# Performance work log

Measured on AMD Instinct MI355X. Metric: run time of the kernel, lower is better.

Reference implementation:

```python
import jax, jax.numpy as jnp
import numpy as np
import math

EMBED = 1024
HEADS = 16
HEAD_DIM = EMBED // HEADS
B, Hh, Ww = 256, 10, 10
MAX_POS = 100


def setup_inputs() -> dict:
    key = jax.random.key(0)
    ks = jax.random.split(key, 10)
    s = 1.0 / math.sqrt(EMBED)
    return {
        "x": jax.random.normal(ks[0], (B, EMBED, Hh, Ww), dtype=jnp.float32),
        "Wq": jax.random.uniform(ks[1], (EMBED, EMBED), jnp.float32, -s, s),
        "bq": jax.random.uniform(ks[2], (EMBED,), jnp.float32, -s, s),
        "Wk": jax.random.uniform(ks[3], (EMBED, EMBED), jnp.float32, -s, s),
        "bk": jax.random.uniform(ks[4], (EMBED,), jnp.float32, -s, s),
        "Wv": jax.random.uniform(ks[5], (EMBED, EMBED), jnp.float32, -s, s),
        "bv": jax.random.uniform(ks[6], (EMBED,), jnp.float32, -s, s),
        "Wo": jax.random.uniform(ks[7], (EMBED, EMBED), jnp.float32, -s, s),
        "bo": jax.random.uniform(ks[8], (EMBED,), jnp.float32, -s, s),
        "pos_encoding": jax.random.normal(ks[9], (MAX_POS, EMBED), dtype=jnp.float32),
    }


def reference(x, Wq, bq, Wk, bk, Wv, bv, Wo, bo, pos_encoding):
    # x: [B, E, H, W]
    b, e, h, w = x.shape
    s = h * w  # seq_len
    scale = math.sqrt(HEAD_DIM)
    x_flat = x.reshape(b, e, s).transpose(0, 2, 1)  # [B, S, E]
    x_flat = x_flat + pos_encoding[:s][None]  # broadcast over batch
    q = x_flat @ Wq + bq
    k = x_flat @ Wk + bk
    v = x_flat @ Wv + bv
    # [B, H, S, D]
    q = q.reshape(b, s, HEADS, HEAD_DIM).transpose(0, 2, 1, 3)
    k = k.reshape(b, s, HEADS, HEAD_DIM).transpose(0, 2, 1, 3)
    v = v.reshape(b, s, HEADS, HEAD_DIM).transpose(0, 2, 1, 3)
    scores = jnp.einsum('bhqd,bhkd->bhqk', q, k) / scale
    attn = jax.nn.softmax(scores, axis=-1)  # dropout = identity (eval)
    attended = jnp.einsum('bhqk,bhkd->bhqd', attn, v)
    attended = attended.transpose(0, 2, 1, 3).reshape(b, s, e)
    out = attended @ Wo + bo
    out = out.transpose(0, 2, 1).reshape(b, e, h, w)
    return out, attn
```

## Files before the change

### kernel.cpp

```cpp
#include <hip/hip_runtime.h>

typedef unsigned short u16;
typedef __attribute__((ext_vector_type(8))) short short8;
typedef __attribute__((ext_vector_type(4))) float f32x4;

#define BATCH 256
#define S_LEN 100
#define EMB   1024
#define NHEAD 16
#define HDIM  64

__device__ __forceinline__ float b2f(u16 h) {
  union { unsigned u; float f; } v; v.u = ((unsigned)h) << 16; return v.f;
}
__device__ __forceinline__ u16 f2bf(float f) {
  union { float f; unsigned u; } v; v.f = f;
  unsigned r = v.u + 0x7fffu + ((v.u >> 16) & 1u);
  return (u16)(r >> 16);
}

__device__ __forceinline__ void gld_lds16(const u16* g, u16* l) {
  __builtin_amdgcn_global_load_lds((const __attribute__((address_space(1))) void*)g,
                                   (__attribute__((address_space(3))) void*)l,
                                   16, 0, 0);
}

__global__ __launch_bounds__(256) void w_xpose(
    const float* __restrict__ Wq, const float* __restrict__ Wk,
    const float* __restrict__ Wv, const float* __restrict__ Wo,
    u16* __restrict__ WtQ, u16* __restrict__ WtK,
    u16* __restrict__ WtV, u16* __restrict__ WtO)
{
  __shared__ u16 tile[64 * 73];
  int z = blockIdx.z;
  const float* W = (z == 0) ? Wq : (z == 1) ? Wk : (z == 2) ? Wv : Wo;
  u16* Wt        = (z == 0) ? WtQ : (z == 1) ? WtK : (z == 2) ? WtV : WtO;
  int k0 = blockIdx.x * 64, n0 = blockIdx.y * 64;
  for (int idx = threadIdx.x; idx < 4096; idx += 256) {
    int r = idx >> 6, c = idx & 63;
    tile[r * 73 + c] = f2bf(W[(size_t)(k0 + r) * EMB + n0 + c]);
  }
  __syncthreads();
  for (int idx = threadIdx.x; idx < 4096; idx += 256) {
    int c = idx >> 6, r = idx & 63;
    Wt[(size_t)(n0 + c) * EMB + k0 + r] = tile[r * 73 + c];
  }
}

__global__ __launch_bounds__(256) void xpose_pos(
    const float* __restrict__ x, const float* __restrict__ pos, u16* __restrict__ xT)
{
  __shared__ float tile[64 * 105];
  int e0 = blockIdx.x * 64;
  int b  = blockIdx.y;
  const float* xb = x + (size_t)b * EMB * S_LEN;
  for (int idx = threadIdx.x; idx < 6400; idx += 256) {
    int i = idx / 100, s = idx - i * 100;
    tile[i * 105 + s] = xb[(size_t)(e0 + i) * S_LEN + s];
  }
  __syncthreads();
  for (int idx = threadIdx.x; idx < 6400; idx += 256) {
    int s = idx >> 6, i = idx & 63;
    float v = tile[i * 105 + s] + pos[(size_t)s * EMB + e0 + i];
    xT[(size_t)b * (S_LEN * EMB) + (size_t)s * EMB + e0 + i] = f2bf(v);
  }
}

__global__ __launch_bounds__(256) void out_xpose(
    const u16* __restrict__ tmp, float* __restrict__ out)
{
  __shared__ u16 tile[100 * 73];
  int e0 = blockIdx.x * 64;
  int b  = blockIdx.y;
  for (int idx = threadIdx.x; idx < 6400; idx += 256) {
    int s = idx >> 6, i = idx & 63;
    tile[s * 73 + i] = tmp[(size_t)b * (S_LEN * EMB) + (size_t)s * EMB + e0 + i];
  }
  __syncthreads();
  for (int idx = threadIdx.x; idx < 6400; idx += 256) {
    int i = idx / 100, s = idx - i * 100;
    out[((size_t)b * EMB + e0 + i) * S_LEN + s] = b2f(tile[s * 73 + i]);
  }
}

__global__ __launch_bounds__(256) void gemm_bt(
    const u16* __restrict__ A,
    const u16* __restrict__ Bt0, const u16* __restrict__ Bt1, const u16* __restrict__ Bt2,
    const float* __restrict__ bias0, const float* __restrict__ bias1, const float* __restrict__ bias2,
    u16* __restrict__ C0, u16* __restrict__ C1, u16* __restrict__ C2,
    int Kd, int Nd)
{
  __shared__ u16 lA[128 * 64];
  __shared__ u16 lB[128 * 64];
  int z = blockIdx.z;
  const u16* Bt     = (z == 0) ? Bt0 : (z == 1) ? Bt1 : Bt2;
  const float* bias = (z == 0) ? bias0 : (z == 1) ? bias1 : bias2;
  u16* C            = (z == 0) ? C0 : (z == 1) ? C1 : C2;

  const int tid  = threadIdx.x;
  const int wave = tid >> 6, lane = tid & 63;
  const int quad = lane >> 4, l16 = lane & 15;
  const int m0 = blockIdx.x * 128, n0 = blockIdx.y * 128;
  const int wm = (wave >> 1) * 64, wn = (wave & 1) * 64;

  f32x4 acc[4][4] = {};

  for (int k0 = 0; k0 < Kd; k0 += 64) {
#pragma unroll
    for (int i = 0; i < 4; ++i) {
      int slot = (i * 4 + wave) * 64 + lane;
      int row  = slot >> 3;
      int jg   = ((slot & 7) ^ (row & 7)) << 3;
      gld_lds16(A  + (size_t)(m0 + row) * Kd + k0 + jg, lA + (i * 4 + wave) * 512);
      gld_lds16(Bt + (size_t)(n0 + row) * Kd + k0 + jg, lB + (i * 4 + wave) * 512);
    }
    __syncthreads();
#pragma unroll
    for (int kk = 0; kk < 64; kk += 32) {
      short8 af[4], bf[4];
#pragma unroll
      for (int mi = 0; mi < 4; ++mi) {
        int row = wm + mi * 16 + l16;
        af[mi] = *(const short8*)(lA + row * 64 + ((((kk >> 3) + quad) ^ (row & 7)) << 3));
      }
#pragma unroll
      for (int ni = 0; ni < 4; ++ni) {
        int row = wn + ni * 16 + l16;
        bf[ni] = *(const short8*)(lB + row * 64 + ((((kk >> 3) + quad) ^ (row & 7)) << 3));
      }
#pragma unroll
      for (int mi = 0; mi < 4; ++mi)
#pragma unroll
        for (int ni = 0; ni < 4; ++ni)
          acc[mi][ni] = __builtin_amdgcn_mfma_f32_16x16x32_bf16(af[mi], bf[ni], acc[mi][ni], 0, 0, 0);
    }
    __syncthreads();
  }

#pragma unroll
  for (int ni = 0; ni < 4; ++ni) {
    int col = n0 + wn + ni * 16 + l16;
    float bv = bias[col];
#pragma unroll
    for (int mi = 0; mi < 4; ++mi) {
#pragma unroll
      for (int r = 0; r < 4; ++r) {
        int row = m0 + wm + mi * 16 + quad * 4 + r;
        C[(size_t)row * Nd + col] = f2bf(acc[mi][ni][r] + bv);
      }
    }
  }
}

__global__ __launch_bounds__(256) void attn_kernel(
    const u16* __restrict__ Q, const u16* __restrict__ Kb, const u16* __restrict__ V,
    float* __restrict__ attn_out, u16* __restrict__ attended)
{
  __shared__ u16 sQK[112 * 64 * 2];
  __shared__ __align__(16) char smemB[100 * 105 * 4];
  __shared__ float sRed[256];

  u16* sQ   = sQK;
  u16* sK   = sQK + 112 * 64;
  u16* sP   = sQK;
  float* sS = (float*)smemB;
  u16* sVt  = (u16*)smemB;

  const int bh = blockIdx.x;
  const int b = bh >> 4, h = bh & 15;
  const int tid = threadIdx.x;
  const int wave = tid >> 6, lane = tid & 63;
  const int quad = lane >> 4, l16 = lane & 15;
  const size_t qbase = (size_t)b * S_LEN * EMB + h * HDIM;

  uint4 vr0, vr1, vr2, vr3 = make_uint4(0, 0, 0, 0);
  {
    int c0 = tid, c1 = tid + 256, c2 = tid + 512;
    vr0 = *(const uint4*)(V + qbase + (size_t)(c0 >> 3) * EMB + ((c0 & 7) << 3));
    vr1 = *(const uint4*)(V + qbase + (size_t)(c1 >> 3) * EMB + ((c1 & 7) << 3));
    vr2 = *(const uint4*)(V + qbase + (size_t)(c2 >> 3) * EMB + ((c2 & 7) << 3));
    if (tid < 32) {
      int c3 = tid + 768;
      vr3 = *(const uint4*)(V + qbase + (size_t)(c3 >> 3) * EMB + ((c3 & 7) << 3));
    }
  }

  for (int c = tid; c < 896; c += 256) {
    int s = c >> 3, j = c & 7;
    int jg = (j ^ (s & 7)) << 3;
    uint4 qv = make_uint4(0, 0, 0, 0), kv = make_uint4(0, 0, 0, 0);
    if (s < S_LEN) {
      qv = *(const uint4*)(Q  + qbase + (size_t)s * EMB + jg);
      kv = *(const uint4*)(Kb + qbase + (size_t)s * EMB + jg);
    }
    *(uint4*)(sQ + c * 8) = qv;
    *(uint4*)(sK + c * 8) = kv;
  }
  __syncthreads();

  for (int t = wave; t < 49; t += 4) {
    int mi = t / 7, ni = t - mi * 7;
    f32x4 acc = {0.f, 0.f, 0.f, 0.f};
#pragma unroll
    for (int kk = 0; kk < 64; kk += 32) {
      int rq = mi * 16 + l16, rk = ni * 16 + l16;
      int cix = (kk >> 3) + quad;
      short8 a  = *(const short8*)(sQ + rq * 64 + ((cix ^ (rq & 7)) << 3));
      short8 bb = *(const short8*)(sK + rk * 64 + ((cix ^ (rk & 7)) << 3));
      acc = __builtin_amdgcn_mfma_f32_16x16x32_bf16(a, bb, acc, 0, 0, 0);
    }
    int col = ni * 16 + l16;
#pragma unroll
    for (int r = 0; r < 4; ++r) {
      int row = mi * 16 + quad * 4 + r;
      if (row < S_LEN && col < S_LEN) sS[row * 105 + col] = acc[r] * 0.125f;
    }
  }
  __syncthreads();

  for (int i = tid; i < 192; i += 256)
    *(uint4*)(sP + (100 + (i >> 4)) * 128 + ((i & 15) << 3)) = make_uint4(0, 0, 0, 0);

  if (tid < 200) {
    int row = tid >> 1, half = tid & 1;
    float* Srow = sS + row * 105;
    int c0 = half * 50, c1 = c0 + 50;
    float m0 = -1e30f, m1 = -1e30f;
    for (int c = c0; c < c1; c += 2) {
      m0 = fmaxf(m0, Srow[c]);
      m1 = fmaxf(m1, Srow[c + 1]);
    }
    sRed[tid] = fmaxf(m0, m1);
  }
  __syncthreads();
  if (tid < 200) {
    int row = tid >> 1, half = tid & 1;
    float* Srow = sS + row * 105;
    float mxv = fmaxf(sRed[row * 2], sRed[row * 2 + 1]);
    int c0 = half * 50, c1 = c0 + 50;
    float s0 = 0.f, s1 = 0.f;
    for (int c = c0; c < c1; c += 2) {
      float e0 = __expf(Srow[c] - mxv);
      float e1 = __expf(Srow[c + 1] - mxv);
      Srow[c] = e0; Srow[c + 1] = e1;
      s0 += e0; s1 += e1;
    }
    sRed[tid] = s0 + s1;
  }
  __syncthreads();
  if (tid < 200) {
    int row = tid >> 1, half = tid & 1;
    float* Srow = sS + row * 105;
    u16* Prow = sP + row * 128;
    int rs = row & 7;
    float inv = 1.f / (sRed[row * 2] + sRed[row * 2 + 1]);
    int c0 = half * 50, c1 = c0 + 50;
    for (int c = c0; c < c1; ++c) {
      float p = Srow[c] * inv;
      Srow[c] = p;
      Prow[(((c >> 3) ^ rs) << 3) + (c & 7)] = f2bf(p);
    }
    if (half == 1) {
      for (int c = S_LEN; c < 128; ++c)
        Prow[(((c >> 3) ^ rs) << 3) + (c & 7)] = 0;
    }
  }
  __syncthreads();

  {
    float* ao = attn_out + (size_t)bh * (S_LEN * S_LEN);
    for (int i = tid; i < S_LEN * S_LEN; i += 256) {
      int r = i / 100, c = i - r * 100;
      ao[i] = sS[r * 105 + c];
    }
  }
  __syncthreads();

  for (int i = tid; i < 1024; i += 256)
    *(uint4*)(sVt + i * 8) = make_uint4(0, 0, 0, 0);
  __syncthreads();
  {
    const u16* p0 = (const u16*)&vr0;
    const u16* p1 = (const u16*)&vr1;
    const u16* p2 = (const u16*)&vr2;
    const u16* p3 = (const u16*)&vr3;
    int c0 = tid, c1 = tid + 256, c2 = tid + 512, c3 = tid + 768;
#pragma unroll
    for (int j = 0; j < 8; ++j) {
      int s, d;
      s = c0 >> 3; d = ((c0 & 7) << 3) + j;
      sVt[d * 128 + (((s >> 3) ^ (d & 7)) << 3) + (s & 7)] = p0[j];
      s = c1 >> 3; d = ((c1 & 7) << 3) + j;
      sVt[d * 128 + (((s >> 3) ^ (d & 7)) << 3) + (s & 7)] = p1[j];
      s = c2 >> 3; d = ((c2 & 7) << 3) + j;
      sVt[d * 128 + (((s >> 3) ^ (d & 7)) << 3) + (s & 7)] = p2[j];
      if (tid < 32) {
        s = c3 >> 3; d = ((c3 & 7) << 3) + j;
        sVt[d * 128 + (((s >> 3) ^ (d & 7)) << 3) + (s & 7)] = p3[j];
      }
    }
  }
  __syncthreads();

  for (int t = wave; t < 28; t += 4) {
    int mi = t >> 2, ni = t & 3;
    f32x4 acc = {0.f, 0.f, 0.f, 0.f};
#pragma unroll
    for (int kk = 0; kk < 128; kk += 32) {
      int rp = mi * 16 + l16, rv = ni * 16 + l16;
      int cix = (kk >> 3) + quad;
      short8 a  = *(const short8*)(sP  + rp * 128 + ((cix ^ (rp & 7)) << 3));
      short8 bb = *(const short8*)(sVt + rv * 128 + ((cix ^ (rv & 7)) << 3));
      acc = __builtin_amdgcn_mfma_f32_16x16x32_bf16(a, bb, acc, 0, 0, 0);
    }
    int col = ni * 16 + l16;
#pragma unroll
    for (int r = 0; r < 4; ++r) {
      int row = mi * 16 + quad * 4 + r;
      if (row < S_LEN)
        attended[((size_t)b * S_LEN + row) * EMB + h * HDIM + col] = f2bf(acc[r]);
    }
  }
}

extern "C" void kernel_launch(void* const* d_in, const int* in_sizes, int n_in,
                              void* d_out, int out_size, void* d_ws, size_t ws_size,
                              hipStream_t stream) {
  const float* x   = (const float*)d_in[0];
  const float* Wq  = (const float*)d_in[1];
  const float* bq  = (const float*)d_in[2];
  const float* Wk  = (const float*)d_in[3];
  const float* bk  = (const float*)d_in[4];
  const float* Wv  = (const float*)d_in[5];
  const float* bv  = (const float*)d_in[6];
  const float* Wo  = (const float*)d_in[7];
  const float* bo  = (const float*)d_in[8];
  const float* pos = (const float*)d_in[9];

  float* out  = (float*)d_out;
  float* attn = out + (size_t)BATCH * EMB * S_LEN;

  const size_t MTOT = (size_t)BATCH * S_LEN;
  u16* ws   = (u16*)d_ws;
  u16* xT   = ws;
  u16* Qb   = ws + MTOT * EMB;
  u16* Kbuf = ws + 2 * MTOT * EMB;
  u16* Vb   = ws + 3 * MTOT * EMB;
  u16* WtQ  = ws + 4 * MTOT * EMB;
  u16* WtK  = WtQ + (size_t)EMB * EMB;
  u16* WtV  = WtK + (size_t)EMB * EMB;
  u16* WtO  = WtV + (size_t)EMB * EMB;
  u16* attended = xT;
  u16* tmp      = Qb;

  w_xpose<<<dim3(16, 16, 4), 256, 0, stream>>>(Wq, Wk, Wv, Wo, WtQ, WtK, WtV, WtO);
  xpose_pos<<<dim3(16, BATCH), 256, 0, stream>>>(x, pos, xT);
  gemm_bt<<<dim3(200, 8, 3), 256, 0, stream>>>(xT, WtQ, WtK, WtV, bq, bk, bv,
                                               Qb, Kbuf, Vb, EMB, EMB);
  attn_kernel<<<dim3(BATCH * NHEAD), 256, 0, stream>>>(Qb, Kbuf, Vb, attn, attended);
  gemm_bt<<<dim3(200, 8, 1), 256, 0, stream>>>(attended, WtO, WtO, WtO, bo, bo, bo,
                                               tmp, tmp, tmp, EMB, EMB);
  out_xpose<<<dim3(16, BATCH), 256, 0, stream>>>(tmp, out);
}
```

Before: 810.1 us.

## Replace GEMM with 256x256-tile double-buffered pipelined kernel

New measurement: 758.7 us. 1.07x faster.

```diff
diff --git a/kernel.cpp b/kernel.cpp
--- a/kernel.cpp
+++ b/kernel.cpp
@@ -24,6 +24,8 @@
                                    (__attribute__((address_space(3))) void*)l,
                                    16, 0, 0);
 }
+
+#define MFMA16(a, b, c) __builtin_amdgcn_mfma_f32_16x16x32_bf16(a, b, c, 0, 0, 0)
 
 __global__ __launch_bounds__(256) void w_xpose(
     const float* __restrict__ Wq, const float* __restrict__ Wk,
@@ -83,16 +85,15 @@
   }
 }
 
-__global__ __launch_bounds__(256) void gemm_bt(
+__global__ __launch_bounds__(512) void gemm256(
     const u16* __restrict__ A,
     const u16* __restrict__ Bt0, const u16* __restrict__ Bt1, const u16* __restrict__ Bt2,
     const float* __restrict__ bias0, const float* __restrict__ bias1, const float* __restrict__ bias2,
-    u16* __restrict__ C0, u16* __restrict__ C1, u16* __restrict__ C2,
-    int Kd, int Nd)
+    u16* __restrict__ C0, u16* __restrict__ C1, u16* __restrict__ C2)
 {
-  __shared__ u16 lA[128 * 64];
-  __shared__ u16 lB[128 * 64];
-  int z = blockIdx.z;
+  __shared__ u16 lds[2][2][16384];
+
+  const int z = blockIdx.z;
   const u16* Bt     = (z == 0) ? Bt0 : (z == 1) ? Bt1 : Bt2;
   const float* bias = (z == 0) ? bias0 : (z == 1) ? bias1 : bias2;
   u16* C            = (z == 0) ? C0 : (z == 1) ? C1 : C2;
@@ -100,56 +101,97 @@
   const int tid  = threadIdx.x;
   const int wave = tid >> 6, lane = tid & 63;
   const int quad = lane >> 4, l16 = lane & 15;
-  const int m0 = blockIdx.x * 128, n0 = blockIdx.y * 128;
-  const int wm = (wave >> 1) * 64, wn = (wave & 1) * 64;
-
-  f32x4 acc[4][4] = {};
-
-  for (int k0 = 0; k0 < Kd; k0 += 64) {
-#pragma unroll
-    for (int i = 0; i < 4; ++i) {
-      int slot = (i * 4 + wave) * 64 + lane;
-      int row  = slot >> 3;
-      int jg   = ((slot & 7) ^ (row & 7)) << 3;
-      gld_lds16(A  + (size_t)(m0 + row) * Kd + k0 + jg, lA + (i * 4 + wave) * 512);
-      gld_lds16(Bt + (size_t)(n0 + row) * Kd + k0 + jg, lB + (i * 4 + wave) * 512);
-    }
-    __syncthreads();
-#pragma unroll
-    for (int kk = 0; kk < 64; kk += 32) {
-      short8 af[4], bf[4];
-#pragma unroll
-      for (int mi = 0; mi < 4; ++mi) {
-        int row = wm + mi * 16 + l16;
-        af[mi] = *(const short8*)(lA + row * 64 + ((((kk >> 3) + quad) ^ (row & 7)) << 3));
+  const int m0 = blockIdx.x * 256, n0 = blockIdx.y * 256;
+  const int WM = (wave >> 2) * 128, WN = (wave & 3) * 64;
+
+  const int rq8  = tid >> 3;
+  const int jg   = ((tid & 7) ^ (rq8 & 7)) << 3;
+  const int hi96 = (tid >= 256) ? 96 : 0;
+  const int aw   = (wave & 3) * 8 + (wave >> 2) * 128;
+  const size_t aBase = (size_t)(m0 + rq8 + hi96) * EMB + jg;
+  const size_t bBase = (size_t)(n0 + rq8) * EMB + jg;
+
+#define STB(nb, u, k1) gld_lds16(Bt + bBase + (size_t)((u) * 64) * EMB + (k1), \
+                                 &lds[nb][1][(u) * 4096 + wave * 512])
+#define STA(nb, p, k1) gld_lds16(A + aBase + (size_t)((p) * 32) * EMB + (k1), \
+                                 &lds[nb][0][((p) * 32 + aw) * 64])
+#define GATE(N) { asm volatile("s_waitcnt vmcnt(" #N ")" ::: "memory"); \
+                  __builtin_amdgcn_s_barrier(); }
+
+  f32x4 acc[8][4] = {};
+
+  STB(0, 0, 0); STB(0, 1, 0); STB(0, 2, 0); STB(0, 3, 0);
+  STA(0, 0, 0); STA(0, 1, 0); STA(0, 2, 0); STA(0, 3, 0);
+  GATE(3);
+
+  const int swz = l16 & 7;
+  const int cA  = (quad ^ swz) << 3;
+  const int cB  = ((quad + 4) ^ swz) << 3;
+
+#define PH(q, STAGES, GATE_) { \
+    short8 aF[2][2], bF[2][4]; \
+    aF[0][0] = *(const short8*)(a0 + (2 * (q)) * 1024); \
+    aF[0][1] = *(const short8*)(a1 + (2 * (q)) * 1024); \
+    aF[1][0] = *(const short8*)(a0 + (2 * (q) + 1) * 1024); \
+    aF[1][1] = *(const short8*)(a1 + (2 * (q) + 1) * 1024); \
+    _Pragma("unroll") \
+    for (int ni = 0; ni < 4; ++ni) { \
+      bF[0][ni] = *(const short8*)(b0 + ni * 1024); \
+      bF[1][ni] = *(const short8*)(b1 + ni * 1024); \
+    } \
+    STAGES; \
+    __builtin_amdgcn_s_setprio(1); \
+    _Pragma("unroll") \
+    for (int kh = 0; kh < 2; ++kh) { \
+      _Pragma("unroll") \
+      for (int ni = 0; ni < 4; ++ni) { \
+        acc[2 * (q)][ni]     = MFMA16(aF[0][kh], bF[kh][ni], acc[2 * (q)][ni]); \
+        acc[2 * (q) + 1][ni] = MFMA16(aF[1][kh], bF[kh][ni], acc[2 * (q) + 1][ni]); \
+      } \
+    } \
+    __builtin_amdgcn_s_setprio(0); \
+    GATE_; \
+  }
+
+  for (int t = 0; t < 16; ++t) {
+    const int cb = t & 1, nb = cb ^ 1;
+    const u16* lA_ = lds[cb][0];
+    const u16* lB_ = lds[cb][1];
+    const u16* a0 = lA_ + (WM + l16) * 64 + cA;
+    const u16* a1 = lA_ + (WM + l16) * 64 + cB;
+    const u16* b0 = lB_ + (WN + l16) * 64 + cA;
+    const u16* b1 = lB_ + (WN + l16) * 64 + cB;
+    const int k1 = (t + 1) << 6;
+    if (t < 15) {
+      PH(0, { STB(nb, 0, k1); STB(nb, 1, k1); }, GATE(4));
+      PH(1, { STB(nb, 2, k1); STB(nb, 3, k1); }, GATE(5));
+      PH(2, { STA(nb, 0, k1); STA(nb, 1, k1); }, GATE(6));
+      PH(3, { STA(nb, 2, k1); STA(nb, 3, k1); }, GATE(3));
+    } else {
+      PH(0, { (void)0; }, GATE(2));
+      PH(1, { (void)0; }, GATE(1));
+      PH(2, { (void)0; }, GATE(0));
+      PH(3, { (void)0; }, { (void)0; });
+    }
+  }
+
+#pragma unroll
+  for (int ni = 0; ni < 4; ++ni) {
+    int col = n0 + WN + ni * 16 + l16;
+    float bv = bias[col];
+#pragma unroll
+    for (int mi = 0; mi < 8; ++mi) {
+#pragma unroll
+      for (int r = 0; r < 4; ++r) {
+        int row = m0 + WM + mi * 16 + quad * 4 + r;
+        C[(size_t)row * EMB + col] = f2bf(acc[mi][ni][r] + bv);
       }
-#pragma unroll
-      for (int ni = 0; ni < 4; ++ni) {
-        int row = wn + ni * 16 + l16;
-        bf[ni] = *(const short8*)(lB + row * 64 + ((((kk >> 3) + quad) ^ (row & 7)) << 3));
-      }
-#pragma unroll
-      for (int mi = 0; mi < 4; ++mi)
-#pragma unroll
-        for (int ni = 0; ni < 4; ++ni)
-          acc[mi][ni] = __builtin_amdgcn_mfma_f32_16x16x32_bf16(af[mi], bf[ni], acc[mi][ni], 0, 0, 0);
-    }
-    __syncthreads();
-  }
-
-#pragma unroll
-  for (int ni = 0; ni < 4; ++ni) {
-    int col = n0 + wn + ni * 16 + l16;
-    float bv = bias[col];
-#pragma unroll
-    for (int mi = 0; mi < 4; ++mi) {
-#pragma unroll
-      for (int r = 0; r < 4; ++r) {
-        int row = m0 + wm + mi * 16 + quad * 4 + r;
-        C[(size_t)row * Nd + col] = f2bf(acc[mi][ni][r] + bv);
-      }
-    }
-  }
+    }
+  }
+#undef PH
+#undef STB
+#undef STA
+#undef GATE
 }
 
 __global__ __launch_bounds__(256) void attn_kernel(
@@ -355,10 +397,10 @@
 
   w_xpose<<<dim3(16, 16, 4), 256, 0, stream>>>(Wq, Wk, Wv, Wo, WtQ, WtK, WtV, WtO);
   xpose_pos<<<dim3(16, BATCH), 256, 0, stream>>>(x, pos, xT);
-  gemm_bt<<<dim3(200, 8, 3), 256, 0, stream>>>(xT, WtQ, WtK, WtV, bq, bk, bv,
-                                               Qb, Kbuf, Vb, EMB, EMB);
+  gemm256<<<dim3(100, 4, 3), 512, 0, stream>>>(xT, WtQ, WtK, WtV, bq, bk, bv,
+                                               Qb, Kbuf, Vb);
   attn_kernel<<<dim3(BATCH * NHEAD), 256, 0, stream>>>(Qb, Kbuf, Vb, attn, attended);
-  gemm_bt<<<dim3(200, 8, 1), 256, 0, stream>>>(attended, WtO, WtO, WtO, bo, bo, bo,
-                                               tmp, tmp, tmp, EMB, EMB);
+  gemm256<<<dim3(100, 4, 1), 512, 0, stream>>>(attended, WtO, WtO, WtO, bo, bo, bo,
+                                               tmp, tmp, tmp);
   out_xpose<<<dim3(16, BATCH), 256, 0, stream>>>(tmp, out);
 }
```
